# Performance work log

Hardware: AMD Instinct MI355X
Metric: run time of the kernel (lower is better)

The kernel has to match this reference:

```python
import jax, jax.numpy as jnp
import numpy as np
from jax import lax

NUM_SUPERNODES = 1024
KNN_K = 16
MIN_GRIPPER = 16
MIN_MASK = 8
GRIP_START = 0
GRIP_RADIUS = 0.1
NEG_INF = -jnp.inf


def _take(a, idx):
    return jnp.take_along_axis(a, idx, axis=1)


def _scatter_or(idx, keep, Bf, N):
    # OR `keep` into a fresh [Bf,N] bool mask at positions idx (mirrors torch scatter_)
    b = jnp.arange(Bf)[:, None]
    return jnp.zeros((Bf, N), dtype=bool).at[b, idx].max(keep)


def _cdist(a, b):
    # a [B,M,3], b [B,N,3] -> [B,M,N] euclidean
    d2 = (jnp.sum(a * a, -1)[:, :, None] + jnp.sum(b * b, -1)[:, None, :]
          - 2.0 * jnp.einsum('bmd,bnd->bmn', a, b))
    return jnp.sqrt(jnp.maximum(d2, 0.0))


def _sample_supernodes(xyz, valid, state, mask_id, extra_scores, global_scores):
    Bf, N, _ = xyz.shape
    M = NUM_SUPERNODES
    valid = valid.astype(bool)
    row_has_valid = valid.any(axis=1)
    first_valid = jnp.argmax(valid, axis=1).astype(jnp.int32)  # [Bf]

    # ---- gripper quota: nearest points to gripper xyz (within radius if any) ----
    k_grip = min(MIN_GRIPPER, M)
    gxyz = state[:, GRIP_START:GRIP_START + 3]
    gdist = jnp.linalg.norm(xyz - gxyz[:, None, :], axis=-1)  # [Bf,N]
    in_radius = gdist <= GRIP_RADIUS
    has_radius = (valid & in_radius).any(axis=1, keepdims=True)
    eligible = valid & (in_radius | ~has_radius)
    dist_rank = jnp.where(eligible, gdist, jnp.inf)
    neg_vals, grip_idx = lax.top_k(-dist_rank, k_grip)
    grip_vals = -neg_vals
    grip_keep = jnp.isfinite(grip_vals) & row_has_valid[:, None]
    head_idx = jnp.where(grip_keep, grip_idx, first_valid[:, None])
    head_bucket = jnp.where(grip_keep, 1, -1)
    selected = _scatter_or(grip_idx, grip_keep, Bf, N)

    remaining = M - k_grip
    # ---- mask-instance quota: one point per mask id (dedup via sort) ----
    mask_cand = valid & ~selected
    sentinel = jnp.iinfo(mask_id.dtype).max
    mask_key = jnp.where(mask_cand, mask_id, sentinel)
    sort_idx = jnp.argsort(mask_key, axis=1)
    sorted_valid = _take(mask_cand, sort_idx)
    sorted_mask = _take(mask_id, sort_idx)
    first_for_id = jnp.concatenate(
        [sorted_valid[:, :1],
         sorted_valid[:, 1:] & (sorted_mask[:, 1:] != sorted_mask[:, :-1])], axis=1)
    pos = jnp.arange(N, dtype=jnp.float32)[None, :]
    mask_scores = jnp.where(first_for_id, -pos, NEG_INF)
    mask_vals, mask_pos = lax.top_k(mask_scores, remaining)
    mask_idx = _take(sort_idx, mask_pos)
    mask_keep = jnp.isfinite(mask_vals) & row_has_valid[:, None]
    selected_after_mask = selected | _scatter_or(mask_idx, mask_keep, Bf, N)

    # ---- extra random mask supernodes to guarantee min_mask quota ----
    k_extra = min(MIN_MASK, remaining)
    es = jnp.where(valid & ~selected_after_mask, extra_scores, NEG_INF)
    extra_vals, extra_idx = lax.top_k(es, k_extra)
    extra_keep = jnp.isfinite(extra_vals) & row_has_valid[:, None]
    use_extra = ~mask_keep[:, :k_extra] & extra_keep
    mask_idx = mask_idx.at[:, :k_extra].set(
        jnp.where(use_extra, extra_idx, mask_idx[:, :k_extra]))
    mask_keep = mask_keep.at[:, :k_extra].set(mask_keep[:, :k_extra] | use_extra)

    # ---- global random fill ----
    selected_for_global = selected | _scatter_or(mask_idx, mask_keep, Bf, N)
    gs = jnp.where(valid & ~selected_for_global, global_scores, NEG_INF)
    gvals, gidx = lax.top_k(gs, remaining)
    gkeep = jnp.isfinite(gvals) & row_has_valid[:, None]
    fill_idx = jnp.where(mask_keep, mask_idx,
                         jnp.where(gkeep, gidx, first_valid[:, None]))
    fill_bucket = jnp.where(mask_keep, 2, jnp.where(gkeep, 0, -1))

    out_idx = jnp.concatenate([head_idx, fill_idx], axis=1)
    out_bucket = jnp.concatenate([head_bucket, fill_bucket], axis=1)
    out_valid = _take(valid, out_idx) & row_has_valid[:, None]
    out_bucket = jnp.where(out_valid, out_bucket, -1)
    return out_idx, out_valid, out_bucket


def setup_inputs() -> dict:
    key = jax.random.key(0)
    ks = jax.random.split(key, 6)
    Bf, N, C = 8, 16384, 64
    return {
        'x': jax.random.normal(ks[0], (Bf, N, C), dtype=jnp.float32),
        'xyz': jax.random.normal(ks[1], (Bf, N, 3), dtype=jnp.float32),
        'valid': jnp.ones((Bf, N), dtype=bool),
        'state': jax.random.normal(ks[2], (Bf, 8), dtype=jnp.float32),
        'mask_id': jax.random.randint(ks[3], (Bf, N), 0, 32, dtype=jnp.int32),
        'extra_scores': jax.random.uniform(ks[4], (Bf, N), dtype=jnp.float32),
        'global_scores': jax.random.uniform(ks[5], (Bf, N), dtype=jnp.float32),
    }


def reference(x, xyz, valid, state, mask_id, extra_scores, global_scores):
    Bf, N, C = x.shape
    out_idx, out_valid, out_bucket = _sample_supernodes(
        xyz, valid, state, mask_id, extra_scores, global_scores)
    # gather_points
    supernode_xyz = _take(xyz, out_idx[:, :, None].repeat(3, axis=2))  # [Bf,M,3]
    # build_knn_neighbors: masked cdist + topk smallest
    dist = _cdist(supernode_xyz.astype(jnp.float32), xyz.astype(jnp.float32))
    dist = jnp.where(valid.astype(bool)[:, None, :], dist, jnp.inf)
    neg_vals, neighbor_idx = lax.top_k(-dist, KNN_K)
    neighbor_mask = jnp.isfinite(-neg_vals)  # [Bf,M,K]
    # gather_neighbors
    b = jnp.arange(Bf)[:, None, None]
    neighbor_feats = x[b, neighbor_idx]  # [Bf,M,K,C]
    return (neighbor_feats, supernode_xyz, neighbor_mask,
            out_idx, out_valid, out_bucket)
```

## Files before the change

### kernel.cpp

```cpp
#include <hip/hip_runtime.h>
#include <math.h>

typedef unsigned long long u64;
typedef unsigned int u32;

#define BF 8
#define NPTS 16384
#define M_SN 1024
#define CCH 64
#define KNN 16
#define NTHR1 1024
#define KPER 16
#define TBL 4096
#define CCAP 2048
#define REM 1008

constexpr size_t O0 = 0;
constexpr size_t O1 = 8388608;
constexpr size_t O2 = 8413184;
constexpr size_t O3 = 8544256;
constexpr size_t O4 = 8552448;
constexpr size_t O5 = 8560640;

#define PW_OFF ((size_t)256)
#define PW_BYTES ((size_t)BF * NPTS * 16)
#define SEG1_BYTES ((size_t)BF * M_SN * KNN * 8)

__device__ __forceinline__ bool is_valid_el(const void* vp, int mode, long long i) {
  if (mode == 1) return ((const unsigned char*)vp)[i] != 0;
  if (mode == 2) return ((const float*)vp)[i] != 0.0f;
  return ((const int*)vp)[i] != 0;
}

__device__ __forceinline__ u32 desc_enc(float f) {
  u32 u = __float_as_uint(f);
  u32 s = (u & 0x80000000u) ? ~u : (u | 0x80000000u);
  return ~s;
}
__device__ __forceinline__ bool enc_finite(u32 d) {
  u32 s = ~d;
  u32 u = (s & 0x80000000u) ? (s & 0x7FFFFFFFu) : ~s;
  return (u & 0x7F800000u) != 0x7F800000u;
}

__device__ __forceinline__ u64 wave_min_u64(u64 v) {
#pragma unroll
  for (int d = 32; d >= 1; d >>= 1) {
    u32 lo = __shfl_xor((u32)(v & 0xFFFFFFFFu), d, 64);
    u32 hi = __shfl_xor((u32)(v >> 32), d, 64);
    u64 o = ((u64)hi << 32) | lo;
    if (o < v) v = o;
  }
  return v;
}

__device__ __forceinline__ u64 block_min_u64(u64 v, u64* red16, int t) {
  v = wave_min_u64(v);
  if ((t & 63) == 0) red16[t >> 6] = v;
  __syncthreads();
  if (t < 64) {
    u64 x = red16[t & 15];
    x = wave_min_u64(x);
    if (t == 0) red16[0] = x;
  }
  __syncthreads();
  u64 r = red16[0];
  __syncthreads();
  return r;
}

__device__ __forceinline__ int block_excl_scan(int val, int* scanb, int t, int* tot) {
  int incl = val;
#pragma unroll
  for (int d = 1; d < 64; d <<= 1) {
    int v = __shfl_up(incl, d, 64);
    if ((t & 63) >= d) incl += v;
  }
  if ((t & 63) == 63) scanb[t >> 6] = incl;
  __syncthreads();
  if (t < 64) {
    int ws = (t < 16) ? scanb[t] : 0;
#pragma unroll
    for (int d = 1; d < 16; d <<= 1) {
      int v = __shfl_up(ws, d, 64);
      if ((t & 63) >= d) ws += v;
    }
    if (t < 16) scanb[16 + t] = ws;
  }
  __syncthreads();
  int wv = t >> 6;
  int base = (wv == 0) ? 0 : scanb[16 + wv - 1];
  *tot = scanb[16 + 15];
  int r = base + incl - val;
  __syncthreads();
  return r;
}

template<bool ASC, bool SHIFTBIN>
__device__ __forceinline__ void topk_select(const u32* ek, const u32* bk, u32 cmask,
    int Twant, int* table, u64* cand, int* scanb, int* sh, int* outArr, int t) {
  for (int j = t; j < TBL; j += NTHR1) table[j] = 0;
  if (t == 6) sh[6] = 0x7FFFFFFF;
  if (t == 7) sh[7] = 1;
  __syncthreads();
#pragma unroll
  for (int k = 0; k < KPER; k++) {
    if ((cmask >> k) & 1u) {
      int bin = SHIFTBIN ? (int)(ek[k] >> 20) : (int)bk[k];
      atomicAdd(&table[bin], 1);
    }
  }
  __syncthreads();
  int c_[4]; int c4 = 0;
#pragma unroll
  for (int q = 0; q < 4; q++) { c_[q] = table[4 * t + q]; c4 += c_[q]; }
  int htot;
  int cum = block_excl_scan(c4, scanb, t, &htot);
  const int T = min(Twant, htot);
  int e_ = cum;
#pragma unroll
  for (int q = 0; q < 4; q++) {
    int nx = e_ + c_[q];
    if (T > 0 && e_ < T && nx >= T) atomicMin(&sh[6], 4 * t + q);
    table[4 * t + q] = e_;
    e_ = nx;
  }
  __syncthreads();
  if (T <= 0) return;
  const int B = sh[6];
#pragma unroll
  for (int k = 0; k < KPER; k++) {
    if ((cmask >> k) & 1u) {
      int bin = SHIFTBIN ? (int)(ek[k] >> 20) : (int)bk[k];
      if (bin <= B) {
        int pos = atomicAdd(&table[bin], 1);
        if (pos < CCAP)
          cand[pos] = ((u64)ek[k] << 32) | ((u64)(u32)bin << 14) | (u32)(k * NTHR1 + t);
      }
    }
  }
  __syncthreads();
  const int nc = table[B];
  if (nc <= CCAP) {
    for (int c = t; c < nc; c += NTHR1) {
      u64 key = cand[c];
      int bin = (int)((key >> 14) & 0xFFFu);
      int s = bin ? table[bin - 1] : 0;
      int e2 = table[bin];
      int r = s;
      for (int j = s; j < e2; j++) r += (cand[j] < key);
      if (r < T) {
        u32 enc = (u32)(key >> 32);
        int ix = (int)(key & 0x3FFFu);
        bool fin = ASC ? (enc < 0x7F800000u) : enc_finite(enc);
        outArr[r] = fin ? ix : (ix | (int)0x80000000);
      }
    }
  } else {
    if (t == 0) sh[7] = 0;
  }
  __syncthreads();
}

__global__ void detect_valid(const unsigned* __restrict__ w, int nwords, int* __restrict__ flag) {
  __shared__ int cls;
  int t = threadIdx.x;
  if (t == 0) cls = 0;
  __syncthreads();
  int local = 0;
  for (int i = t; i < nwords; i += blockDim.x) {
    unsigned v = w[i];
    if (v == 0x3F800000u) local = 2;
    else if (v != 0u && v != 1u) local = max(local, 1);
  }
  if (local) atomicMax(&cls, local);
  __syncthreads();
  if (t == 0) flag[0] = cls;
}

__global__ __launch_bounds__(1024)
void sample_kernel(const float* __restrict__ xyz, const void* __restrict__ validp,
                   const float* __restrict__ state, const int* __restrict__ mask_id,
                   const float* __restrict__ extra, const float* __restrict__ glob,
                   int vwords, float4* __restrict__ pw, float* __restrict__ out) {
  __shared__ u64 red16[16];
  __shared__ int table[TBL];
  __shared__ int scanb[32];
  __shared__ int mpick[REM];
  __shared__ u64 cand[CCAP];
  __shared__ int gsorted[REM];
  __shared__ int head_i[16];
  __shared__ int head_bk[16];
  __shared__ int sh[8];

  const int b = blockIdx.x, t = threadIdx.x;
  const float* xyzb = xyz + (size_t)b * NPTS * 3;
  const int* midb = mask_id + (size_t)b * NPTS;
  const float* exb = extra + (size_t)b * NPTS;
  const float* glb = glob + (size_t)b * NPTS;

  if (t < 8) sh[t] = 0;
  if (t == 1) sh[1] = 0x7FFFFFFF;
  if (t < 16) gsorted[t] = -1;
  __syncthreads();

  {
    const unsigned* w = (const unsigned*)validp;
    int local = 0;
    for (int i = t; i < vwords; i += NTHR1) {
      unsigned vv = w[i];
      if (vv == 0x3F800000u) local = 2;
      else if (vv != 0u && vv != 1u) local = max(local, 1);
    }
    if (local) atomicMax(&sh[3], local);
  }
  __syncthreads();
  const int vmode = sh[3];

  u32 vbits = 0;
#pragma unroll
  for (int k = 0; k < KPER; k++) {
    int i = k * NTHR1 + t;
    if (is_valid_el(validp, vmode, (long long)b * NPTS + i)) vbits |= 1u << k;
  }
  if (vbits) {
    atomicOr(&sh[0], 1);
    atomicMin(&sh[1], (__ffs(vbits) - 1) * NTHR1 + t);
  }

  float gx = state[b * 8 + 0], gy = state[b * 8 + 1], gz = state[b * 8 + 2];
  float gd[KPER];
  u32 inr = 0;
#pragma unroll
  for (int k = 0; k < KPER; k++) {
    int i = k * NTHR1 + t;
    float px = xyzb[3 * i], py = xyzb[3 * i + 1], pz = xyzb[3 * i + 2];
    float dx = px - gx, dy = py - gy, dz = pz - gz;
    float d = sqrtf((dx * dx + dy * dy) + dz * dz);
    gd[k] = d;
    bool vb = (vbits >> k) & 1u;
    if (vb && d <= 0.1f) inr |= 1u << k;
    if (pw) {
      float sb = __fadd_rn(__fadd_rn(__fmul_rn(px, px), __fmul_rn(py, py)), __fmul_rn(pz, pz));
      pw[(size_t)b * NPTS + i] = make_float4(px, py, pz, vb ? sb : INFINITY);
    }
  }
  if (inr) atomicOr(&sh[2], 1);
  __syncthreads();

  const int rhv = sh[0];
  const int first_valid = rhv ? sh[1] : 0;
  const u32 elig = vbits & (sh[2] ? inr : 0xFFFFu);
  u32 sel = 0;

  {
    u32 ek[KPER];
#pragma unroll
    for (int k = 0; k < KPER; k++) ek[k] = __float_as_uint(gd[k]);
    topk_select<true, true>(ek, nullptr, elig, 16, table, cand, scanb, sh, gsorted, t);
    if (sh[7]) {
      if (t < 16) {
        int g = gsorted[t];
        head_i[t] = (g >= 0) ? g : first_valid;
        head_bk[t] = (g >= 0) ? 1 : -1;
      }
      __syncthreads();
      for (int j = 0; j < 16; j++) {
        if (head_bk[j] == 1) {
          int ix = head_i[j];
          if ((ix & (NTHR1 - 1)) == t) sel |= 1u << (ix >> 10);
        }
      }
    } else {
      for (int it = 0; it < 16; ++it) {
        u64 best = ~0ull;
#pragma unroll
        for (int k = 0; k < KPER; k++) {
          if (((elig >> k) & 1u) && !((sel >> k) & 1u)) {
            u64 key = ((u64)__float_as_uint(gd[k]) << 32) | (u32)(k * NTHR1 + t);
            if (key < best) best = key;
          }
        }
        u64 w = block_min_u64(best, red16, t);
        bool keep = (w >> 32) < 0x7F800000ull;
        int idx = (int)(w & 0xFFFFFFFFu);
        if (t == 0) { head_i[it] = keep ? idx : first_valid; head_bk[it] = keep ? 1 : -1; }
        if (keep && (idx & (NTHR1 - 1)) == t) sel |= 1u << (idx >> 10);
      }
      __syncthreads();
    }
  }

  for (int j = t; j < TBL; j += NTHR1) table[j] = 0x7FFFFFFF;
  __syncthreads();
#pragma unroll
  for (int k = 0; k < KPER; k++) {
    if (((vbits >> k) & 1u) && !((sel >> k) & 1u)) {
      int i = k * NTHR1 + t;
      int id = midb[i];
      if ((u32)id < TBL) atomicMin(&table[id], i);
    }
  }
  __syncthreads();
  int cnt = 0;
#pragma unroll
  for (int q = 0; q < 4; q++) cnt += (table[4 * t + q] != 0x7FFFFFFF);
  int mtot;
  int excl = block_excl_scan(cnt, scanb, t, &mtot);
  {
    int pos = excl;
#pragma unroll
    for (int q = 0; q < 4; q++) {
      int v = table[4 * t + q];
      if (v != 0x7FFFFFFF) { if (pos < REM) mpick[pos] = v; pos++; }
    }
  }
  __syncthreads();
  const int nm = min(mtot, REM);
  for (int j = 0; j < nm; j++) {
    int p = mpick[j];
    if ((p & (NTHR1 - 1)) == t) sel |= 1u << (p >> 10);
  }

  u32 extra_used = 0;
  if (nm < 8 && rhv) {
    u32 extrbits = 0;
    for (int j = 0; j < 8; j++) {
      u64 best = ~0ull;
#pragma unroll
      for (int k = 0; k < KPER; k++) {
        if (((vbits >> k) & 1u) && !((sel >> k) & 1u) && !((extrbits >> k) & 1u)) {
          int i = k * NTHR1 + t;
          u64 key = ((u64)desc_enc(exb[i]) << 32) | (u32)i;
          if (key < best) best = key;
        }
      }
      u64 w = block_min_u64(best, red16, t);
      if (w == ~0ull) break;
      int idx = (int)(w & 0xFFFFFFFFu);
      bool fin = enc_finite((u32)(w >> 32));
      if ((idx & (NTHR1 - 1)) == t) extrbits |= 1u << (idx >> 10);
      if (j >= nm && fin) {
        extra_used |= 1u << j;
        if (t == 0) mpick[j] = idx;
        if ((idx & (NTHR1 - 1)) == t) sel |= 1u << (idx >> 10);
      }
    }
    __syncthreads();
  }

  {
    u32 cbits = vbits & ~sel;
    u32 ek[KPER], bk[KPER];
#pragma unroll
    for (int k = 0; k < KPER; k++) {
      if ((cbits >> k) & 1u) {
        float f = glb[k * NTHR1 + t];
        ek[k] = desc_enc(f);
        float g = fminf(fmaxf(f, 0.0f), 0.99999994f);
        bk[k] = 4095u - (u32)(g * 4096.0f);
      } else { ek[k] = 0xFFFFFFFFu; bk[k] = 4095u; }
    }
    for (int j = t; j < REM; j += NTHR1) gsorted[j] = -1;
    topk_select<false, false>(ek, bk, cbits, REM, table, cand, scanb, sh, gsorted, t);
    if (!sh[7]) {
      u32 gext = 0;
      for (int j = 0; j < REM; j++) {
        u64 best = ~0ull;
#pragma unroll
        for (int k = 0; k < KPER; k++) {
          if (((cbits >> k) & 1u) && !((gext >> k) & 1u)) {
            u64 key = ((u64)ek[k] << 32) | (u32)(k * NTHR1 + t);
            if (key < best) best = key;
          }
        }
        u64 w = block_min_u64(best, red16, t);
        if (w == ~0ull) break;
        int idx = (int)(w & 0xFFFFFFFFu);
        if ((idx & (NTHR1 - 1)) == t) gext |= 1u << (idx >> 10);
        if (t == 0) gsorted[j] = enc_finite((u32)(w >> 32)) ? idx : (idx | (int)0x80000000);
      }
      __syncthreads();
    }
  }

  {
    int slot = t;
    int idx, bucket;
    if (slot < 16) {
      idx = head_i[slot];
      bucket = head_bk[slot];
    } else {
      int jj = slot - 16;
      bool mk = (jj < nm) || (jj < 8 && ((extra_used >> jj) & 1u));
      if (mk) { idx = mpick[jj]; bucket = 2; }
      else {
        int g = gsorted[jj];
        if (rhv && g >= 0) { idx = g; bucket = 0; }
        else { idx = first_valid; bucket = -1; }
      }
    }
    bool ov = rhv && is_valid_el(validp, vmode, (long long)b * NPTS + idx);
    int ob = ov ? bucket : -1;
    size_t o = (size_t)b * M_SN + slot;
    out[O3 + o] = (float)idx;
    out[O4 + o] = ov ? 1.0f : 0.0f;
    out[O5 + o] = (float)ob;
    out[O1 + 3 * o + 0] = xyzb[3 * idx + 0];
    out[O1 + 3 * o + 1] = xyzb[3 * idx + 1];
    out[O1 + 3 * o + 2] = xyzb[3 * idx + 2];
  }
}

#define NTHR2 256
#define SPG 4
#define SNBLK 32

__device__ __forceinline__ float4 load_pt(const float4* pw, const float* xyzb,
    const void* validp, int vmode, long long gbase, int i) {
  if (pw) return pw[gbase + i];
  float px = xyzb[3 * i], py = xyzb[3 * i + 1], pz = xyzb[3 * i + 2];
  bool v = is_valid_el(validp, vmode, gbase + i);
  float sb = __fadd_rn(__fadd_rn(__fmul_rn(px, px), __fmul_rn(py, py)), __fmul_rn(pz, pz));
  return make_float4(px, py, pz, v ? sb : INFINITY);
}

__global__ __launch_bounds__(256)
void knn_kernel(const float* __restrict__ x, const float* __restrict__ xyz,
                const void* __restrict__ validp, const int* __restrict__ flagp,
                const float4* __restrict__ pw, u64* __restrict__ wnws, int nseg,
                float* __restrict__ out) {
  __shared__ u64 wnl[SNBLK * KNN];

  const int b = blockIdx.x >> 5;
  const int snblk = blockIdx.x & 31;
  const int seg = blockIdx.y;
  const int t = threadIdx.x;
  const int g = t >> 5;
  const int sub = t & 31;
  const int lanebase = t & 32;
  const int m0 = snblk * SNBLK + g * SPG;
  const float* xyzb = xyz + (size_t)b * NPTS * 3;
  const long long gbase = (long long)b * NPTS;
  const int vmode = pw ? 0 : flagp[0];

  float a2x[SPG], a2y[SPG], a2z[SPG];
#pragma unroll
  for (int s = 0; s < SPG; s++) {
    int sidx = (int)out[O3 + (size_t)b * M_SN + m0 + s];
    float ax, ay, az;
    if (pw) { float4 c = pw[gbase + sidx]; ax = c.x; ay = c.y; az = c.z; }
    else { ax = xyzb[3 * sidx]; ay = xyzb[3 * sidx + 1]; az = xyzb[3 * sidx + 2]; }
    a2x[s] = ax + ax; a2y[s] = ay + ay; a2z[s] = az + az;
  }

  const int S = NPTS / nseg;
  const int sbeg = seg * S;
  const int NJ = S / 32;

  float ld[SPG]; int li[SPG]; float kq[SPG];

  {
    float4 v = load_pt(pw, xyzb, validp, vmode, gbase, sbeg + sub);
    float qv[SPG]; int qi[SPG];
#pragma unroll
    for (int s = 0; s < SPG; s++) {
      qv[s] = __builtin_fmaf(a2x[s], v.x, __builtin_fmaf(a2y[s], v.y, __builtin_fmaf(a2z[s], v.z, -v.w)));
      qi[s] = sbeg + sub;
    }
#pragma unroll
    for (int p = 0; p < 32; p++) {
      int par;
      if ((p & 1) == 0) par = sub ^ 1;
      else par = (sub == 0 || sub == 31) ? sub : (((sub - 1) ^ 1) + 1);
      bool lo = sub < par;
#pragma unroll
      for (int s = 0; s < SPG; s++) {
        float oq = __shfl(qv[s], par, 32);
        int oi = __shfl(qi[s], par, 32);
        if (par != sub) {
          bool take = lo ? (oq > qv[s]) : (oq < qv[s]);
          if (take) { qv[s] = oq; qi[s] = oi; }
        }
      }
    }
#pragma unroll
    for (int s = 0; s < SPG; s++) { ld[s] = qv[s]; li[s] = qi[s]; kq[s] = __shfl(ld[s], 15, 32); }
  }

  float4 v = load_pt(pw, xyzb, validp, vmode, gbase, sbeg + 32 * (NJ > 1 ? 1 : 0) + sub);
  for (int j = 1; j < NJ; j++) {
    int jn = min(j + 1, NJ - 1);
    float4 vn = load_pt(pw, xyzb, validp, vmode, gbase, sbeg + 32 * jn + sub);
#pragma unroll
    for (int s = 0; s < SPG; s++) {
      float qv = __builtin_fmaf(a2x[s], v.x, __builtin_fmaf(a2y[s], v.y, __builtin_fmaf(a2z[s], v.z, -v.w)));
      u64 bal = __ballot(qv > kq[s]);
      u32 mq = (u32)(bal >> lanebase);
      while (mq) {
        int bb = __ffs(mq) - 1;
        mq &= mq - 1;
        float kd = __shfl(qv, lanebase + bb, 64);
        if (kd > kq[s]) {
          int ki = sbeg + 32 * j + bb;
          bool gt = ld[s] < kd;
          float sd = __shfl_up(ld[s], 1, 32);
          int si = __shfl_up(li[s], 1, 32);
          int pg = __shfl_up(gt ? 1 : 0, 1, 32);
          if (sub == 0) pg = 0;
          ld[s] = gt ? (pg ? sd : kd) : ld[s];
          li[s] = gt ? (pg ? si : ki) : li[s];
          kq[s] = __shfl(ld[s], 15, 32);
        }
      }
    }
    v = vn;
  }

  if (wnws) {
#pragma unroll
    for (int s = 0; s < SPG; s++)
      if (sub < KNN)
        wnws[(((size_t)seg * BF + b) * M_SN + (m0 + s)) * KNN + sub] =
            ((u64)desc_enc(ld[s]) << 32) | (u32)li[s];
    return;
  }

#pragma unroll
  for (int s = 0; s < SPG; s++)
    if (sub < KNN) wnl[(g * SPG + s) * KNN + sub] = ((u64)desc_enc(ld[s]) << 32) | (u32)li[s];
  __syncthreads();
  for (int r = t; r < SNBLK * KNN; r += NTHR2) {
    u64 key = wnl[r];
    int ni = (int)(key & (u64)(NPTS - 1));
    int mm = snblk * SNBLK + (r >> 4);
    size_t o2 = ((size_t)b * M_SN + mm) * KNN + (r & 15);
    out[O2 + o2] = enc_finite((u32)(key >> 32)) ? 1.0f : 0.0f;
    const float4* src = (const float4*)(x + (gbase + ni) * CCH);
    float4* dst = (float4*)(out + O0 + o2 * CCH);
#pragma unroll
    for (int q = 0; q < 16; q++) dst[q] = src[q];
  }
}

#define MSPB 4
__global__ __launch_bounds__(256)
void knn_merge_kernel(const float* __restrict__ x, const u64* __restrict__ wnws,
                      int nseg, float* __restrict__ out) {
  __shared__ u64 keys[MSPB][64];
  __shared__ u64 wsel[MSPB][KNN];
  const int b = blockIdx.x >> 8;
  const int sn0 = (blockIdx.x & 255) * MSPB;
  const int t = threadIdx.x;
  const int s = t >> 6, e = t & 63;
  const int E = nseg * KNN;
  if (e < E) {
    int seg = e >> 4, k = e & 15;
    keys[s][e] = wnws[(((size_t)seg * BF + b) * M_SN + sn0 + s) * KNN + k];
  }
  __syncthreads();
  if (e < E) {
    u64 my = keys[s][e];
    int rk = 0;
    for (int j = 0; j < E; j++) rk += (keys[s][j] < my);
    if (rk < KNN) wsel[s][rk] = my;
  }
  __syncthreads();
  {
    int row = t >> 2, q4 = t & 3;
    u64 key = wsel[row >> 4][row & 15];
    int ni = (int)(key & (u64)(NPTS - 1));
    int mm = sn0 + (row >> 4);
    size_t o2 = ((size_t)b * M_SN + mm) * KNN + (row & 15);
    if (q4 == 0) out[O2 + o2] = enc_finite((u32)(key >> 32)) ? 1.0f : 0.0f;
    const float4* src = (const float4*)(x + ((size_t)b * NPTS + ni) * CCH);
    float4* dst = (float4*)(out + O0 + o2 * CCH);
#pragma unroll
    for (int q = 0; q < 4; q++) dst[q4 * 4 + q] = src[q4 * 4 + q];
  }
}

extern "C" void kernel_launch(void* const* d_in, const int* in_sizes, int n_in,
                              void* d_out, int out_size, void* d_ws, size_t ws_size,
                              hipStream_t stream) {
  const float* x = (const float*)d_in[0];
  const float* xyz = (const float*)d_in[1];
  const void* valid = d_in[2];
  const float* state = (const float*)d_in[3];
  const int* mask_id = (const int*)d_in[4];
  const float* extra = (const float*)d_in[5];
  const float* glob = (const float*)d_in[6];
  float* out = (float*)d_out;
  int* flag = (int*)d_ws;
  const int vwords = in_sizes[2] / 4;

  float4* pw = nullptr;
  u64* wnws = nullptr;
  int nseg = 1;
  if (ws_size >= PW_OFF + PW_BYTES) pw = (float4*)((char*)d_ws + PW_OFF);
  if (pw && ws_size >= PW_OFF + PW_BYTES + 4 * SEG1_BYTES) {
    nseg = 4; wnws = (u64*)((char*)d_ws + PW_OFF + PW_BYTES);
  } else if (pw && ws_size >= PW_OFF + PW_BYTES + 2 * SEG1_BYTES) {
    nseg = 2; wnws = (u64*)((char*)d_ws + PW_OFF + PW_BYTES);
  }

  if (!pw)
    detect_valid<<<1, 1024, 0, stream>>>((const unsigned*)valid, vwords, flag);
  sample_kernel<<<BF, NTHR1, 0, stream>>>(xyz, valid, state, mask_id, extra, glob,
                                          vwords, pw, out);
  dim3 kg(BF * 32, nseg);
  knn_kernel<<<kg, NTHR2, 0, stream>>>(x, xyz, valid, flag, pw, wnws, nseg, out);
  if (nseg > 1) knn_merge_kernel<<<BF * 256, NTHR2, 0, stream>>>(x, wnws, nseg, out);
}
```

Baseline: 310.7 us.

## Stage KNN candidate points through shared memory and halve supernodes per warp

Measured after the change: 307.4 us. No clear change (-1.1%).

```diff
diff --git a/kernel.cpp b/kernel.cpp
--- a/kernel.cpp
+++ b/kernel.cpp
@@ -413,27 +413,20 @@
 }
 
 #define NTHR2 256
-#define SPG 4
-#define SNBLK 32
-
-__device__ __forceinline__ float4 load_pt(const float4* pw, const float* xyzb,
-    const void* validp, int vmode, long long gbase, int i) {
-  if (pw) return pw[gbase + i];
-  float px = xyzb[3 * i], py = xyzb[3 * i + 1], pz = xyzb[3 * i + 2];
-  bool v = is_valid_el(validp, vmode, gbase + i);
-  float sb = __fadd_rn(__fadd_rn(__fmul_rn(px, px), __fmul_rn(py, py)), __fmul_rn(pz, pz));
-  return make_float4(px, py, pz, v ? sb : INFINITY);
-}
+#define CH 1024
+#define SPG 2
+#define SNBLK 16
 
 __global__ __launch_bounds__(256)
 void knn_kernel(const float* __restrict__ x, const float* __restrict__ xyz,
                 const void* __restrict__ validp, const int* __restrict__ flagp,
                 const float4* __restrict__ pw, u64* __restrict__ wnws, int nseg,
                 float* __restrict__ out) {
+  __shared__ __align__(16) float4 st[CH];
   __shared__ u64 wnl[SNBLK * KNN];
 
-  const int b = blockIdx.x >> 5;
-  const int snblk = blockIdx.x & 31;
+  const int b = blockIdx.x >> 6;
+  const int snblk = blockIdx.x & 63;
   const int seg = blockIdx.y;
   const int t = threadIdx.x;
   const int g = t >> 5;
@@ -456,65 +449,81 @@
 
   const int S = NPTS / nseg;
   const int sbeg = seg * S;
-  const int NJ = S / 32;
 
   float ld[SPG]; int li[SPG]; float kq[SPG];
 
-  {
-    float4 v = load_pt(pw, xyzb, validp, vmode, gbase, sbeg + sub);
-    float qv[SPG]; int qi[SPG];
-#pragma unroll
-    for (int s = 0; s < SPG; s++) {
-      qv[s] = __builtin_fmaf(a2x[s], v.x, __builtin_fmaf(a2y[s], v.y, __builtin_fmaf(a2z[s], v.z, -v.w)));
-      qi[s] = sbeg + sub;
-    }
-#pragma unroll
-    for (int p = 0; p < 32; p++) {
-      int par;
-      if ((p & 1) == 0) par = sub ^ 1;
-      else par = (sub == 0 || sub == 31) ? sub : (((sub - 1) ^ 1) + 1);
-      bool lo = sub < par;
+  for (int c0 = sbeg; c0 < sbeg + S; c0 += CH) {
+    if (pw) {
+      const float4* src = pw + gbase + c0;
+#pragma unroll
+      for (int qq = 0; qq < CH / NTHR2; qq++) st[t + qq * NTHR2] = src[t + qq * NTHR2];
+    } else {
+      for (int p = t; p < CH; p += NTHR2) {
+        float px = xyzb[3 * (c0 + p)], py = xyzb[3 * (c0 + p) + 1], pz = xyzb[3 * (c0 + p) + 2];
+        bool v = is_valid_el(validp, vmode, gbase + c0 + p);
+        float sb = __fadd_rn(__fadd_rn(__fmul_rn(px, px), __fmul_rn(py, py)), __fmul_rn(pz, pz));
+        st[p] = make_float4(px, py, pz, v ? sb : INFINITY);
+      }
+    }
+    __syncthreads();
+
+    int jstart = 0;
+    if (c0 == sbeg) {
+      float4 v = st[sub];
+      float qv[SPG]; int qi[SPG];
 #pragma unroll
       for (int s = 0; s < SPG; s++) {
-        float oq = __shfl(qv[s], par, 32);
-        int oi = __shfl(qi[s], par, 32);
-        if (par != sub) {
-          bool take = lo ? (oq > qv[s]) : (oq < qv[s]);
-          if (take) { qv[s] = oq; qi[s] = oi; }
+        qv[s] = __builtin_fmaf(a2x[s], v.x, __builtin_fmaf(a2y[s], v.y, __builtin_fmaf(a2z[s], v.z, -v.w)));
+        qi[s] = c0 + sub;
+      }
+#pragma unroll
+      for (int p = 0; p < 32; p++) {
+        int par;
+        if ((p & 1) == 0) par = sub ^ 1;
+        else par = (sub == 0 || sub == 31) ? sub : (((sub - 1) ^ 1) + 1);
+        bool lo = sub < par;
+#pragma unroll
+        for (int s = 0; s < SPG; s++) {
+          float oq = __shfl(qv[s], par, 32);
+          int oi = __shfl(qi[s], par, 32);
+          if (par != sub) {
+            bool take = lo ? (oq > qv[s]) : (oq < qv[s]);
+            if (take) { qv[s] = oq; qi[s] = oi; }
+          }
         }
       }
-    }
-#pragma unroll
-    for (int s = 0; s < SPG; s++) { ld[s] = qv[s]; li[s] = qi[s]; kq[s] = __shfl(ld[s], 15, 32); }
-  }
-
-  float4 v = load_pt(pw, xyzb, validp, vmode, gbase, sbeg + 32 * (NJ > 1 ? 1 : 0) + sub);
-  for (int j = 1; j < NJ; j++) {
-    int jn = min(j + 1, NJ - 1);
-    float4 vn = load_pt(pw, xyzb, validp, vmode, gbase, sbeg + 32 * jn + sub);
-#pragma unroll
-    for (int s = 0; s < SPG; s++) {
-      float qv = __builtin_fmaf(a2x[s], v.x, __builtin_fmaf(a2y[s], v.y, __builtin_fmaf(a2z[s], v.z, -v.w)));
-      u64 bal = __ballot(qv > kq[s]);
-      u32 mq = (u32)(bal >> lanebase);
-      while (mq) {
-        int bb = __ffs(mq) - 1;
-        mq &= mq - 1;
-        float kd = __shfl(qv, lanebase + bb, 64);
-        if (kd > kq[s]) {
-          int ki = sbeg + 32 * j + bb;
-          bool gt = ld[s] < kd;
-          float sd = __shfl_up(ld[s], 1, 32);
-          int si = __shfl_up(li[s], 1, 32);
-          int pg = __shfl_up(gt ? 1 : 0, 1, 32);
-          if (sub == 0) pg = 0;
-          ld[s] = gt ? (pg ? sd : kd) : ld[s];
-          li[s] = gt ? (pg ? si : ki) : li[s];
-          kq[s] = __shfl(ld[s], 15, 32);
+#pragma unroll
+      for (int s = 0; s < SPG; s++) { ld[s] = qv[s]; li[s] = qi[s]; kq[s] = __shfl(ld[s], 15, 32); }
+      jstart = 1;
+    }
+
+#pragma unroll 4
+    for (int j = jstart; j < CH / 32; j++) {
+      float4 v = st[sub + 32 * j];
+#pragma unroll
+      for (int s = 0; s < SPG; s++) {
+        float qv = __builtin_fmaf(a2x[s], v.x, __builtin_fmaf(a2y[s], v.y, __builtin_fmaf(a2z[s], v.z, -v.w)));
+        u64 bal = __ballot(qv > kq[s]);
+        u32 mq = (u32)(bal >> lanebase);
+        while (mq) {
+          int bb = __ffs(mq) - 1;
+          mq &= mq - 1;
+          float kd = __shfl(qv, lanebase + bb, 64);
+          if (kd > kq[s]) {
+            int ki = c0 + 32 * j + bb;
+            bool gt = ld[s] < kd;
+            float sd = __shfl_up(ld[s], 1, 32);
+            int si = __shfl_up(li[s], 1, 32);
+            int pg = __shfl_up(gt ? 1 : 0, 1, 32);
+            if (sub == 0) pg = 0;
+            ld[s] = gt ? (pg ? sd : kd) : ld[s];
+            li[s] = gt ? (pg ? si : ki) : li[s];
+            kq[s] = __shfl(ld[s], 15, 32);
+          }
         }
       }
     }
-    v = vn;
+    __syncthreads();
   }
 
   if (wnws) {
@@ -608,7 +617,7 @@
     detect_valid<<<1, 1024, 0, stream>>>((const unsigned*)valid, vwords, flag);
   sample_kernel<<<BF, NTHR1, 0, stream>>>(xyz, valid, state, mask_id, extra, glob,
                                           vwords, pw, out);
-  dim3 kg(BF * 32, nseg);
+  dim3 kg(BF * 64, nseg);
   knn_kernel<<<kg, NTHR2, 0, stream>>>(x, xyz, valid, flag, pw, wnws, nseg, out);
   if (nseg > 1) knn_merge_kernel<<<BF * 256, NTHR2, 0, stream>>>(x, wnws, nseg, out);
 }
```
